# Performance work log

Hardware: AMD Instinct MI355X
Metric: run time of the kernel (lower is better)

Reference implementation:

```python
import jax, jax.numpy as jnp
import numpy as np
from jax import lax

B, T, D = 8, 4096, 512
UNITS = 512
WINDOW = 2


def setup_inputs() -> dict:
    key = jax.random.key(0)
    k1, k2, k3 = jax.random.split(key, 3)
    x = jax.random.normal(k1, (B, T, D), dtype=jnp.float32)
    # keras kernel shape is (window, 1, input_dim, 3*units); drop the dummy height dim
    kernel = jax.random.uniform(k2, (WINDOW, D, 3 * UNITS), dtype=jnp.float32,
                                minval=-0.05, maxval=0.05)
    bias = jnp.zeros((3 * UNITS,), dtype=jnp.float32)
    return {"x": x, "kernel": kernel, "bias": bias}


def reference(x, kernel, bias):
    window, d_in, u3 = kernel.shape
    units = u3 // 3
    # causal padding: window-1 zeros on the left of the time axis
    xp = jnp.pad(x, ((0, 0), (window - 1, 0), (0, 0)))
    # 1D valid conv -> gates [B, T, 3*units]
    gates = lax.conv_general_dilated(
        xp, kernel, window_strides=(1,), padding='VALID',
        dimension_numbers=('NWC', 'WIO', 'NWC')) + bias
    z = jnp.tanh(gates[..., :units])
    f = jax.nn.sigmoid(gates[..., units:2 * units])
    o = jax.nn.sigmoid(gates[..., 2 * units:])

    # fo-pool recurrence: c_t = f_t * c_{t-1} + (1 - f_t) * z_t ; out_t = o_t * c_t
    def step(c, zfo):
        z_t, f_t, o_t = zfo
        c = f_t * c + (1.0 - f_t) * z_t
        return c, o_t * c

    c0 = jnp.zeros((x.shape[0], units), dtype=x.dtype)
    zT = jnp.swapaxes(z, 0, 1)  # [T, B, U]
    fT = jnp.swapaxes(f, 0, 1)
    oT = jnp.swapaxes(o, 0, 1)
    _, ysT = lax.scan(step, c0, (zT, fT, oT))
    return jnp.swapaxes(ysT, 0, 1)  # [B, T, U] (return_sequences=True)
```

## Files before the change

### kernel.cpp

```cpp
#include <hip/hip_runtime.h>
#include <cstdint>
#include <cstddef>

#define BB   8
#define TT   4096
#define DD   512
#define UU   512
#define NN   1536
#define KK   1024
#define MM   32768
#define NCH  256
#define CHL  16

using bf16x8 = __attribute__((ext_vector_type(8))) __bf16;
using f32x4  = __attribute__((ext_vector_type(4))) float;

__device__ __forceinline__ unsigned short f2bf(float f) {
    unsigned u = __float_as_uint(f);
    u += 0x7fffu + ((u >> 16) & 1u);
    return (unsigned short)(u >> 16);
}
__device__ __forceinline__ float bf2f(unsigned short s) {
    return __uint_as_float(((unsigned)s) << 16);
}
__device__ __forceinline__ float sigf(float x) { return 1.0f / (1.0f + __expf(-x)); }
__device__ __forceinline__ float tanh_(float x) { return 1.0f - 2.0f / (1.0f + __expf(2.0f * x)); }

__device__ __forceinline__ void async16(const void* g, void* l) {
    __builtin_amdgcn_global_load_lds(
        (__attribute__((address_space(1))) void*)g,
        (__attribute__((address_space(3))) void*)l, 16, 0, 0);
}

__global__ void k_prep(const float* __restrict__ x, unsigned short* __restrict__ xpad,
                       const float* __restrict__ kern, unsigned short* __restrict__ kT) {
    int bx = blockIdx.x;
    int by = blockIdx.y;
    int tid = threadIdx.x;
    if (bx < 2049) {
        int q = bx * 256 + tid;
        if (q >= 4097 * 128) return;
        int tp = q >> 7;
        int d  = (q & 127) << 2;
        size_t oi = ((size_t)by * 4097 + tp) * 512 + d;
        ushort4 o;
        if (tp == 0) {
            o.x = o.y = o.z = o.w = 0;
        } else {
            float4 v = *(const float4*)(x + ((size_t)by * 4096 + (tp - 1)) * 512 + d);
            o.x = f2bf(v.x); o.y = f2bf(v.y); o.z = f2bf(v.z); o.w = f2bf(v.w);
        }
        *(ushort4*)(xpad + oi) = o;
    } else {
        __shared__ float tile[32][33];
        int idx = (bx - 2049) * 8 + by;
        int c  = tid & 31;
        int r0 = tid >> 5;
        for (int t8 = 0; t8 < 8; ++t8) {
            int tnum = idx * 8 + t8;
            int k0 = (tnum & 31) * 32;
            int n0 = (tnum >> 5) * 32;
#pragma unroll
            for (int rr = r0; rr < 32; rr += 8)
                tile[rr][c] = kern[(size_t)(k0 + rr) * NN + n0 + c];
            __syncthreads();
#pragma unroll
            for (int rr = r0; rr < 32; rr += 8)
                kT[(size_t)(n0 + rr) * KK + k0 + c] = f2bf(tile[c][rr]);
            __syncthreads();
        }
    }
}

__global__ __launch_bounds__(256) void k_gemm(
    const unsigned short* __restrict__ xpad,
    const unsigned short* __restrict__ kT,
    const float* __restrict__ bias,
    unsigned short* __restrict__ gates)
{
    __shared__ unsigned short As[128 * 64];
    __shared__ unsigned short Bs[128 * 64];
    const int tid  = threadIdx.x;
    const int bi   = blockIdx.x;
    const int xcd  = bi & 7;
    const int loc  = bi >> 3;
    const int mt   = xcd * 32 + loc / 12;
    const int nt   = loc % 12;
    const int m0   = mt * 128;
    const int n0   = nt * 128;
    const int boff = m0 >> 12;
    const size_t abase = (size_t)(m0 + boff) * 512;

    f32x4 acc[4][4] = {};

    const int wid  = tid >> 6;
    const int lane = tid & 63;
    const int wm   = (wid & 1) * 64;
    const int wn   = (wid >> 1) * 64;
    const int lrow = lane & 15;
    const int quad = lane >> 4;

    for (int kk = 0; kk < KK; kk += 64) {
#pragma unroll
        for (int q = 0; q < 4; ++q) {
            int L   = q * 256 + tid;
            int row = L >> 3;
            int sp  = L & 7;
            int sl  = sp ^ (row & 7);
            async16(xpad + abase + (size_t)row * 512 + kk + sl * 8, As + (size_t)L * 8);
            async16(kT + (size_t)(n0 + row) * KK + kk + sl * 8, Bs + (size_t)L * 8);
        }
        __syncthreads();
#pragma unroll
        for (int ks = 0; ks < 2; ++ks) {
            bf16x8 af[4], bfr[4];
#pragma unroll
            for (int i = 0; i < 4; ++i) {
                int row = wm + i * 16 + lrow;
                int sp  = (ks * 4 + quad) ^ (row & 7);
                af[i] = *(const bf16x8*)(As + row * 64 + sp * 8);
            }
#pragma unroll
            for (int j = 0; j < 4; ++j) {
                int row = wn + j * 16 + lrow;
                int sp  = (ks * 4 + quad) ^ (row & 7);
                bfr[j] = *(const bf16x8*)(Bs + row * 64 + sp * 8);
            }
#pragma unroll
            for (int i = 0; i < 4; ++i)
#pragma unroll
                for (int j = 0; j < 4; ++j)
                    acc[i][j] = __builtin_amdgcn_mfma_f32_16x16x32_bf16(af[i], bfr[j], acc[i][j], 0, 0, 0);
        }
        __syncthreads();
    }

#pragma unroll
    for (int j = 0; j < 4; ++j) {
        int col  = n0 + wn + j * 16 + lrow;
        float bv = bias[col];
#pragma unroll
        for (int i = 0; i < 4; ++i) {
            int rbase = m0 + wm + i * 16 + quad * 4;
#pragma unroll
            for (int r = 0; r < 4; ++r) {
                gates[(size_t)(rbase + r) * NN + col] = f2bf(acc[i][j][r] + bv);
            }
        }
    }
}

__global__ __launch_bounds__(128) void k_scanA(const unsigned short* __restrict__ gates,
                        float* __restrict__ Fp, float* __restrict__ Ce) {
    const int chunk = blockIdx.x;
    const int b     = blockIdx.y;
    const int u     = threadIdx.x << 2;
    const size_t g0 = ((size_t)b * TT + (size_t)chunk * CHL) * NN + u;

    float c0 = 0, c1 = 0, c2 = 0, c3 = 0;
    float F0 = 1, F1 = 1, F2 = 1, F3 = 1;

    ushort4 bz[8], bf_[8];
#pragma unroll
    for (int j = 0; j < 8; ++j) {
        bz[j]  = *(const ushort4*)(gates + g0 + (size_t)j * NN);
        bf_[j] = *(const ushort4*)(gates + g0 + (size_t)j * NN + UU);
    }
#pragma unroll
    for (int h = 0; h < 2; ++h) {
        ushort4 nz[8], nf[8];
        if (h == 0) {
#pragma unroll
            for (int j = 0; j < 8; ++j) {
                nz[j] = *(const ushort4*)(gates + g0 + (size_t)(8 + j) * NN);
                nf[j] = *(const ushort4*)(gates + g0 + (size_t)(8 + j) * NN + UU);
            }
        }
#pragma unroll
        for (int j = 0; j < 8; ++j) {
            float f0 = sigf(bf2f(bf_[j].x)), z0 = tanh_(bf2f(bz[j].x));
            float f1 = sigf(bf2f(bf_[j].y)), z1 = tanh_(bf2f(bz[j].y));
            float f2 = sigf(bf2f(bf_[j].z)), z2 = tanh_(bf2f(bz[j].z));
            float f3 = sigf(bf2f(bf_[j].w)), z3 = tanh_(bf2f(bz[j].w));
            c0 = f0 * c0 + (1.0f - f0) * z0; F0 *= f0;
            c1 = f1 * c1 + (1.0f - f1) * z1; F1 *= f1;
            c2 = f2 * c2 + (1.0f - f2) * z2; F2 *= f2;
            c3 = f3 * c3 + (1.0f - f3) * z3; F3 *= f3;
        }
        if (h == 0) {
#pragma unroll
            for (int j = 0; j < 8; ++j) { bz[j] = nz[j]; bf_[j] = nf[j]; }
        }
    }
    size_t ci = ((size_t)b * NCH + chunk) * UU + u;
    *(float4*)(Fp + ci) = make_float4(F0, F1, F2, F3);
    *(float4*)(Ce + ci) = make_float4(c0, c1, c2, c3);
}

__global__ __launch_bounds__(128) void k_scanB(const float* __restrict__ Fp,
                        const float* __restrict__ Ce, float* __restrict__ Cin) {
    int gid = blockIdx.x * 128 + threadIdx.x;
    int bb = gid >> 9;
    int uu = gid & 511;
    size_t base = (size_t)bb * NCH * UU + uu;
    float c = 0.0f;
    for (int k0 = 0; k0 < NCH; k0 += 8) {
        float F[8], E[8];
#pragma unroll
        for (int j = 0; j < 8; ++j) {
            F[j] = Fp[base + (size_t)(k0 + j) * UU];
            E[j] = Ce[base + (size_t)(k0 + j) * UU];
        }
#pragma unroll
        for (int j = 0; j < 8; ++j) {
            Cin[base + (size_t)(k0 + j) * UU] = c;
            c = F[j] * c + E[j];
        }
    }
}

__global__ __launch_bounds__(128) void k_scanC(const unsigned short* __restrict__ gates,
                        const float* __restrict__ Cin, float* __restrict__ out) {
    const int chunk = blockIdx.x;
    const int b     = blockIdx.y;
    const int u     = threadIdx.x << 2;
    const size_t g0 = ((size_t)b * TT + (size_t)chunk * CHL) * NN + u;
    size_t o = ((size_t)b * TT + (size_t)chunk * CHL) * UU + u;

    size_t ci = ((size_t)b * NCH + chunk) * UU + u;
    float4 cv = *(const float4*)(Cin + ci);
    float c0 = cv.x, c1 = cv.y, c2 = cv.z, c3 = cv.w;

    ushort4 bz[4], bf_[4], bo[4];
#pragma unroll
    for (int j = 0; j < 4; ++j) {
        bz[j]  = *(const ushort4*)(gates + g0 + (size_t)j * NN);
        bf_[j] = *(const ushort4*)(gates + g0 + (size_t)j * NN + UU);
        bo[j]  = *(const ushort4*)(gates + g0 + (size_t)j * NN + 2 * UU);
    }
#pragma unroll
    for (int k = 0; k < 4; ++k) {
        ushort4 nz[4], nf[4], no[4];
        if (k < 3) {
#pragma unroll
            for (int j = 0; j < 4; ++j) {
                size_t gg = g0 + (size_t)((k + 1) * 4 + j) * NN;
                nz[j] = *(const ushort4*)(gates + gg);
                nf[j] = *(const ushort4*)(gates + gg + UU);
                no[j] = *(const ushort4*)(gates + gg + 2 * UU);
            }
        }
#pragma unroll
        for (int j = 0; j < 4; ++j) {
            float f0 = sigf(bf2f(bf_[j].x)), z0 = tanh_(bf2f(bz[j].x)), o0 = sigf(bf2f(bo[j].x));
            float f1 = sigf(bf2f(bf_[j].y)), z1 = tanh_(bf2f(bz[j].y)), o1 = sigf(bf2f(bo[j].y));
            float f2 = sigf(bf2f(bf_[j].z)), z2 = tanh_(bf2f(bz[j].z)), o2 = sigf(bf2f(bo[j].z));
            float f3 = sigf(bf2f(bf_[j].w)), z3 = tanh_(bf2f(bz[j].w)), o3 = sigf(bf2f(bo[j].w));
            c0 = f0 * c0 + (1.0f - f0) * z0;
            c1 = f1 * c1 + (1.0f - f1) * z1;
            c2 = f2 * c2 + (1.0f - f2) * z2;
            c3 = f3 * c3 + (1.0f - f3) * z3;
            f32x4 ov = { o0 * c0, o1 * c1, o2 * c2, o3 * c3 };
            __builtin_nontemporal_store(ov, (f32x4*)(out + o));
            o += UU;
        }
        if (k < 3) {
#pragma unroll
            for (int j = 0; j < 4; ++j) { bz[j] = nz[j]; bf_[j] = nf[j]; bo[j] = no[j]; }
        }
    }
}

extern "C" void kernel_launch(void* const* d_in, const int* in_sizes, int n_in,
                              void* d_out, int out_size, void* d_ws, size_t ws_size,
                              hipStream_t stream) {
    const float* x    = (const float*)d_in[0];
    const float* kern = (const float*)d_in[1];
    const float* bias = (const float*)d_in[2];
    float* out = (float*)d_out;
    char* ws = (char*)d_ws;

    unsigned short* xpad  = (unsigned short*)(ws + 0);
    unsigned short* kT    = (unsigned short*)(ws + 33562624);
    unsigned short* gates = (unsigned short*)(ws + 36708352);
    float* Fp  = (float*)(ws + 137371648);
    float* Ce  = (float*)(ws + 141565952);
    float* Cin = (float*)(ws + 145760256);

    hipLaunchKernelGGL(k_prep,  dim3(2049 + 24, 8), dim3(256), 0, stream, x, xpad, kern, kT);
    hipLaunchKernelGGL(k_gemm,  dim3(3072),         dim3(256), 0, stream, xpad, kT, bias, gates);
    hipLaunchKernelGGL(k_scanA, dim3(NCH, BB),      dim3(128), 0, stream, gates, Fp, Ce);
    hipLaunchKernelGGL(k_scanB, dim3(32),           dim3(128), 0, stream, Fp, Ce, Cin);
    hipLaunchKernelGGL(k_scanC, dim3(NCH, BB),      dim3(128), 0, stream, gates, Cin, out);
}
```

Before: 322.3 us.

## Rewrite gate GEMM as 256x256 tile, double-buffered 8-wave pipelined kernel

Replaces the 128x128 single-buffered GEMM tile with a 256x256 tile computed by 8 waves, using a 128 KB LDS double buffer so async global->LDS loads of the next K step overlap with the MFMAs on the current one. Fine-grained phases interleave LDS reads, staging, barriers and s_setprio around MFMA groups, with vmcnt waits instead of full syncthreads. It aims to raise data reuse per tile and hide memory latency in the GEMM, at the cost of more registers and LDS per block, fewer blocks (768), and a fragile hand-scheduled waitcnt/barrier protocol.

```diff
diff --git a/kernel.cpp b/kernel.cpp
--- a/kernel.cpp
+++ b/kernel.cpp
@@ -72,79 +72,140 @@
     }
 }
 
-__global__ __launch_bounds__(256) void k_gemm(
+
+#define STAGE_A(BUF, KT, KH) do { \
+    async16(xpad + abase + (size_t)rowS0 * 512 + ((KT) * 64 + (KH) * 32 + kcS0), \
+            smem + (BUF) * 65536 + (KH) * 16384 + offL0); \
+    async16(xpad + abase + (size_t)rowS1 * 512 + ((KT) * 64 + (KH) * 32 + kcS1), \
+            smem + (BUF) * 65536 + (KH) * 16384 + offL1); \
+} while (0)
+
+#define STAGE_B(BUF, KT, KH) do { \
+    async16(kTg + (size_t)(n0 + rowS0) * 1024 + ((KT) * 64 + (KH) * 32 + kcS0), \
+            smem + (BUF) * 65536 + 32768 + (KH) * 16384 + offL0); \
+    async16(kTg + (size_t)(n0 + rowS1) * 1024 + ((KT) * 64 + (KH) * 32 + kcS1), \
+            smem + (BUF) * 65536 + 32768 + (KH) * 16384 + offL1); \
+} while (0)
+
+#define VM4 asm volatile("s_waitcnt vmcnt(4)" ::: "memory")
+#define VM0 asm volatile("s_waitcnt vmcnt(0)" ::: "memory")
+
+#define LDS_A(BUF, KS, MR) (*(const bf16x8*)(smem + (BUF) * 65536 + (KS) * 16384 + (MR) * 1024 + ldsA))
+#define LDS_B(BUF, KS, NR) (*(const bf16x8*)(smem + (BUF) * 65536 + (KS) * 16384 + (NR) * 1024 + ldsB))
+
+#define PHASE(BUF, MH, KS, LB, STG, VMW) \
+    af[0] = LDS_A(BUF, KS, (MH) * 4 + 0); \
+    af[1] = LDS_A(BUF, KS, (MH) * 4 + 1); \
+    af[2] = LDS_A(BUF, KS, (MH) * 4 + 2); \
+    af[3] = LDS_A(BUF, KS, (MH) * 4 + 3); \
+    if (LB) { \
+        bf[0] = LDS_B(BUF, KS, 0); \
+        bf[1] = LDS_B(BUF, KS, 1); \
+        bf[2] = LDS_B(BUF, KS, 2); \
+        bf[3] = LDS_B(BUF, KS, 3); \
+    } \
+    STG; \
+    __builtin_amdgcn_s_barrier(); \
+    __builtin_amdgcn_s_setprio(1); \
+    acc[(MH)*4+0][0] = __builtin_amdgcn_mfma_f32_16x16x32_bf16(af[0], bf[0], acc[(MH)*4+0][0], 0, 0, 0); \
+    acc[(MH)*4+0][1] = __builtin_amdgcn_mfma_f32_16x16x32_bf16(af[0], bf[1], acc[(MH)*4+0][1], 0, 0, 0); \
+    acc[(MH)*4+0][2] = __builtin_amdgcn_mfma_f32_16x16x32_bf16(af[0], bf[2], acc[(MH)*4+0][2], 0, 0, 0); \
+    acc[(MH)*4+0][3] = __builtin_amdgcn_mfma_f32_16x16x32_bf16(af[0], bf[3], acc[(MH)*4+0][3], 0, 0, 0); \
+    acc[(MH)*4+1][0] = __builtin_amdgcn_mfma_f32_16x16x32_bf16(af[1], bf[0], acc[(MH)*4+1][0], 0, 0, 0); \
+    acc[(MH)*4+1][1] = __builtin_amdgcn_mfma_f32_16x16x32_bf16(af[1], bf[1], acc[(MH)*4+1][1], 0, 0, 0); \
+    acc[(MH)*4+1][2] = __builtin_amdgcn_mfma_f32_16x16x32_bf16(af[1], bf[2], acc[(MH)*4+1][2], 0, 0, 0); \
+    acc[(MH)*4+1][3] = __builtin_amdgcn_mfma_f32_16x16x32_bf16(af[1], bf[3], acc[(MH)*4+1][3], 0, 0, 0); \
+    acc[(MH)*4+2][0] = __builtin_amdgcn_mfma_f32_16x16x32_bf16(af[2], bf[0], acc[(MH)*4+2][0], 0, 0, 0); \
+    acc[(MH)*4+2][1] = __builtin_amdgcn_mfma_f32_16x16x32_bf16(af[2], bf[1], acc[(MH)*4+2][1], 0, 0, 0); \
+    acc[(MH)*4+2][2] = __builtin_amdgcn_mfma_f32_16x16x32_bf16(af[2], bf[2], acc[(MH)*4+2][2], 0, 0, 0); \
+    acc[(MH)*4+2][3] = __builtin_amdgcn_mfma_f32_16x16x32_bf16(af[2], bf[3], acc[(MH)*4+2][3], 0, 0, 0); \
+    acc[(MH)*4+3][0] = __builtin_amdgcn_mfma_f32_16x16x32_bf16(af[3], bf[0], acc[(MH)*4+3][0], 0, 0, 0); \
+    acc[(MH)*4+3][1] = __builtin_amdgcn_mfma_f32_16x16x32_bf16(af[3], bf[1], acc[(MH)*4+3][1], 0, 0, 0); \
+    acc[(MH)*4+3][2] = __builtin_amdgcn_mfma_f32_16x16x32_bf16(af[3], bf[2], acc[(MH)*4+3][2], 0, 0, 0); \
+    acc[(MH)*4+3][3] = __builtin_amdgcn_mfma_f32_16x16x32_bf16(af[3], bf[3], acc[(MH)*4+3][3], 0, 0, 0); \
+    __builtin_amdgcn_s_setprio(0); \
+    VMW; \
+    __builtin_amdgcn_s_barrier();
+
+__global__ __launch_bounds__(512, 2) void k_gemm(
     const unsigned short* __restrict__ xpad,
-    const unsigned short* __restrict__ kT,
+    const unsigned short* __restrict__ kTg,
     const float* __restrict__ bias,
     unsigned short* __restrict__ gates)
 {
-    __shared__ unsigned short As[128 * 64];
-    __shared__ unsigned short Bs[128 * 64];
+    __shared__ char smem[131072];
+
     const int tid  = threadIdx.x;
-    const int bi   = blockIdx.x;
-    const int xcd  = bi & 7;
-    const int loc  = bi >> 3;
-    const int mt   = xcd * 32 + loc / 12;
-    const int nt   = loc % 12;
-    const int m0   = mt * 128;
-    const int n0   = nt * 128;
+    const int wid  = tid >> 6;
+    const int lane = tid & 63;
+    const int wr   = wid >> 2;
+    const int wc   = wid & 3;
+    const int lrow = lane & 15;
+    const int quad = lane >> 4;
+
+    const int bid = blockIdx.x;
+    const int wg  = (bid & 7) * 96 + (bid >> 3);
+    const int mt  = wg / 6;
+    const int nt  = wg % 6;
+    const int m0  = mt * 256;
+    const int n0  = nt * 256;
     const int boff = m0 >> 12;
     const size_t abase = (size_t)(m0 + boff) * 512;
 
-    f32x4 acc[4][4] = {};
-
-    const int wid  = tid >> 6;
-    const int lane = tid & 63;
-    const int wm   = (wid & 1) * 64;
-    const int wn   = (wid >> 1) * 64;
-    const int lrow = lane & 15;
-    const int quad = lane >> 4;
-
-    for (int kk = 0; kk < KK; kk += 64) {
-#pragma unroll
-        for (int q = 0; q < 4; ++q) {
-            int L   = q * 256 + tid;
-            int row = L >> 3;
-            int sp  = L & 7;
-            int sl  = sp ^ (row & 7);
-            async16(xpad + abase + (size_t)row * 512 + kk + sl * 8, As + (size_t)L * 8);
-            async16(kT + (size_t)(n0 + row) * KK + kk + sl * 8, Bs + (size_t)L * 8);
-        }
-        __syncthreads();
-#pragma unroll
-        for (int ks = 0; ks < 2; ++ks) {
-            bf16x8 af[4], bfr[4];
-#pragma unroll
-            for (int i = 0; i < 4; ++i) {
-                int row = wm + i * 16 + lrow;
-                int sp  = (ks * 4 + quad) ^ (row & 7);
-                af[i] = *(const bf16x8*)(As + row * 64 + sp * 8);
-            }
-#pragma unroll
-            for (int j = 0; j < 4; ++j) {
-                int row = wn + j * 16 + lrow;
-                int sp  = (ks * 4 + quad) ^ (row & 7);
-                bfr[j] = *(const bf16x8*)(Bs + row * 64 + sp * 8);
-            }
-#pragma unroll
-            for (int i = 0; i < 4; ++i)
-#pragma unroll
-                for (int j = 0; j < 4; ++j)
-                    acc[i][j] = __builtin_amdgcn_mfma_f32_16x16x32_bf16(af[i], bfr[j], acc[i][j], 0, 0, 0);
-        }
-        __syncthreads();
-    }
-
-#pragma unroll
-    for (int j = 0; j < 4; ++j) {
-        int col  = n0 + wn + j * 16 + lrow;
+    const int off0 = (wid * 2 + 0) * 1024 + lane * 16;
+    const int off1 = (wid * 2 + 1) * 1024 + lane * 16;
+    const int ln0 = off0 >> 7, ln1 = off1 >> 7;
+    const int g80 = ((off0 >> 4) & 7) ^ (ln0 & 7);
+    const int g81 = ((off1 >> 4) & 7) ^ (ln1 & 7);
+    const int offL0 = off0, offL1 = off1;
+    const int rowS0 = ln0 * 2 + (g80 >> 2), rowS1 = ln1 * 2 + (g81 >> 2);
+    const int kcS0 = (g80 & 3) * 8,         kcS1 = (g81 & 3) * 8;
+
+    const int lh  = lrow >> 1;
+    const int g8f = ((lrow & 1) * 4 + quad) ^ lh;
+    const int ldsA = (wr * 64 + lh) * 128 + g8f * 16;
+    const int ldsB = 32768 + (wc * 32 + lh) * 128 + g8f * 16;
+
+    f32x4 acc[8][4] = {};
+    bf16x8 af[4], bf[4];
+
+    STAGE_A(0, 0, 0); STAGE_B(0, 0, 0); STAGE_A(0, 0, 1); STAGE_B(0, 0, 1);
+    VM4;
+    __builtin_amdgcn_s_barrier();
+
+    for (int i = 0; i < 7; ++i) {
+        const int t1 = 2 * i + 1;
+        const int t2 = 2 * i + 2;
+        PHASE(0, 0, 0, 1, STAGE_A(1, t1, 0), (void)0)
+        PHASE(0, 1, 0, 0, STAGE_B(1, t1, 0), VM4)
+        PHASE(0, 0, 1, 1, STAGE_A(1, t1, 1), (void)0)
+        PHASE(0, 1, 1, 0, STAGE_B(1, t1, 1), VM4)
+        PHASE(1, 0, 0, 1, STAGE_A(0, t2, 0), (void)0)
+        PHASE(1, 1, 0, 0, STAGE_B(0, t2, 0), VM4)
+        PHASE(1, 0, 1, 1, STAGE_A(0, t2, 1), (void)0)
+        PHASE(1, 1, 1, 0, STAGE_B(0, t2, 1), VM4)
+    }
+    {
+        PHASE(0, 0, 0, 1, STAGE_A(1, 15, 0), (void)0)
+        PHASE(0, 1, 0, 0, STAGE_B(1, 15, 0), VM4)
+        PHASE(0, 0, 1, 1, STAGE_A(1, 15, 1), (void)0)
+        PHASE(0, 1, 1, 0, STAGE_B(1, 15, 1), VM4)
+        PHASE(1, 0, 0, 1, (void)0, (void)0)
+        PHASE(1, 1, 0, 0, (void)0, VM0)
+        PHASE(1, 0, 1, 1, (void)0, (void)0)
+        PHASE(1, 1, 1, 0, (void)0, (void)0)
+    }
+
+#pragma unroll
+    for (int n = 0; n < 4; ++n) {
+        int col  = n0 + wc * 64 + n * 16 + lrow;
         float bv = bias[col];
 #pragma unroll
-        for (int i = 0; i < 4; ++i) {
-            int rbase = m0 + wm + i * 16 + quad * 4;
+        for (int m = 0; m < 8; ++m) {
+            int rbase = m0 + wr * 128 + m * 16 + quad * 4;
 #pragma unroll
             for (int r = 0; r < 4; ++r) {
-                gates[(size_t)(rbase + r) * NN + col] = f2bf(acc[i][j][r] + bv);
+                gates[(size_t)(rbase + r) * NN + col] = f2bf(acc[m][n][r] + bv);
             }
         }
     }
@@ -288,7 +349,7 @@
     float* Cin = (float*)(ws + 145760256);
 
     hipLaunchKernelGGL(k_prep,  dim3(2049 + 24, 8), dim3(256), 0, stream, x, xpad, kern, kT);
-    hipLaunchKernelGGL(k_gemm,  dim3(3072),         dim3(256), 0, stream, xpad, kT, bias, gates);
+    hipLaunchKernelGGL(k_gemm,  dim3(768),          dim3(512), 0, stream, xpad, kT, bias, gates);
     hipLaunchKernelGGL(k_scanA, dim3(NCH, BB),      dim3(128), 0, stream, gates, Fp, Ce);
     hipLaunchKernelGGL(k_scanB, dim3(32),           dim3(128), 0, stream, Fp, Ce, Cin);
     hipLaunchKernelGGL(k_scanC, dim3(NCH, BB),      dim3(128), 0, stream, gates, Cin, out);
```

After: 318.0 us. About the same (-1.3%).
